# Kernel tuning notes

Hardware: AMD Instinct MI355X
Metric: run time of the kernel (lower is better)

The kernel has to match this reference:

```python
import jax, jax.numpy as jnp
import numpy as np

IN_F = 4096
OUT_F = 4096
RANK = 128  # config.group_size doubles as LoRA rank
B, S = 8, 16


def setup_inputs() -> dict:
    key = jax.random.key(0)
    k_x, k_wq, k_s, k_a, k_b, k_bias = jax.random.split(key, 6)
    x = jax.random.normal(k_x, (B, S, IN_F), dtype=jnp.float32)
    # 4-bit signed quantized weights stored as int8 in torch; int32 here, values in [-8, 7]
    weight_quantized = jax.random.randint(k_wq, (OUT_F, IN_F), -8, 8, dtype=jnp.int32)
    weight_scale = jax.random.uniform(k_s, (OUT_F,), dtype=jnp.float32, minval=0.01, maxval=0.1)
    # kaiming_uniform-ish init for lora_A; lora_B nonzero here so grads flow in tests
    bound = 1.0 / np.sqrt(IN_F)
    lora_A = jax.random.uniform(k_a, (IN_F, RANK), dtype=jnp.float32, minval=-bound, maxval=bound)
    lora_B = jax.random.normal(k_b, (RANK, OUT_F), dtype=jnp.float32) * 0.01
    bias = jax.random.normal(k_bias, (OUT_F,), dtype=jnp.float32) * 0.01
    return {"x": x, "weight_quantized": weight_quantized, "weight_scale": weight_scale,
            "lora_A": lora_A, "lora_B": lora_B, "bias": bias}


def reference(x, weight_quantized, weight_scale, lora_A, lora_B, bias):
    # dequantize: per-output-row scale (out, in)
    weight_dequant = weight_quantized.astype(x.dtype) * weight_scale[:, None]
    # low-rank LoRA update (in, out); square layer so broadcast-add is elementwise
    lora_weight = lora_A @ lora_B
    weight = weight_dequant + lora_weight
    # F.linear: x @ weight.T + bias
    out = jnp.einsum('bsi,oi->bso', x, weight) + bias
    return out
```

## Files before the change

kernel.cpp:

```cpp
#include <hip/hip_runtime.h>
#include <hip/hip_bf16.h>

typedef __attribute__((ext_vector_type(8))) short short8;
typedef __attribute__((ext_vector_type(4))) float f32x4;
using u16 = unsigned short;
using u32 = unsigned int;

#define IN_F 4096
#define OUT_F 4096
#define RANK 128

__device__ inline u32 packi(int a, int b) {
    float fa = (float)a, fb = (float)b;
    return (__builtin_bit_cast(u32, fa) >> 16) |
           (__builtin_bit_cast(u32, fb) & 0xFFFF0000u);
}
__device__ inline u32 packf(float a, float b) {
    u32 ua = __builtin_bit_cast(u32, a);
    u32 ub = __builtin_bit_cast(u32, b);
    ua = (ua + 0x7FFFu + ((ua >> 16) & 1u)) >> 16;
    ub = (ub + 0x7FFFu + ((ub >> 16) & 1u));
    return ua | (ub & 0xFFFF0000u);
}
__device__ inline u16 f2bf(float f) {
    u32 u = __builtin_bit_cast(u32, f);
    u = (u + 0x7FFFu + ((u >> 16) & 1u)) >> 16;
    return (u16)u;
}

#define WS_Y 0
#define WS_YP 65536
#define WS_XB (WS_YP + 1048576)
#define WS_BT (WS_XB + 1048576)
#define WS_AT (WS_BT + 1048576)
#define WS_PART (WS_AT + 1048576)

__global__ __launch_bounds__(512) void prep1_kernel(
    const float* __restrict__ x, const float* __restrict__ A,
    const float* __restrict__ B, u16* __restrict__ xb,
    u16* __restrict__ at, u16* __restrict__ bt) {
    __shared__ float tile[64 * 33];
    int bid = blockIdx.x, tid = threadIdx.x;
    if (bid < 128) {
        const f32x4* xv = (const f32x4*)x;
        int vi = bid * 1024 + tid * 2;
        f32x4 a = xv[vi], b = xv[vi + 1];
        union { u32 u[4]; short8 s; } p;
        p.u[0] = packf(a[0], a[1]); p.u[1] = packf(a[2], a[3]);
        p.u[2] = packf(b[0], b[1]); p.u[3] = packf(b[2], b[3]);
        *(short8*)(xb + (size_t)vi * 4) = p.s;
    } else if (bid < 384) {
        int b2 = bid - 128, kt = b2 >> 2, rt = b2 & 3;
        int k0 = kt * 64, r0 = rt * 32;
        for (int u = tid; u < 2048; u += 512) {
            int row = u >> 5, c = u & 31;
            tile[row * 33 + c] = A[(size_t)(k0 + row) * RANK + r0 + c];
        }
        __syncthreads();
        for (int u = tid; u < 2048; u += 512) {
            int rr = u >> 6, k = u & 63;
            at[(size_t)(r0 + rr) * IN_F + k0 + k] = f2bf(tile[k * 33 + rr]);
        }
    } else {
        int b2 = bid - 384, rt = b2 >> 7, ot = b2 & 127;
        int r0 = rt * 64, o0 = ot * 32;
        for (int u = tid; u < 2048; u += 512) {
            int row = u >> 5, c = u & 31;
            tile[row * 33 + c] = B[(size_t)(r0 + row) * OUT_F + o0 + c];
        }
        __syncthreads();
        for (int u = tid; u < 2048; u += 512) {
            int oo = u >> 6, k = u & 63;
            bt[(size_t)(o0 + oo) * RANK + r0 + k] = f2bf(tile[k * 33 + oo]);
        }
    }
}

__global__ __launch_bounds__(512) void prep2_kernel(
    const u16* __restrict__ xb, const u16* __restrict__ at,
    float* __restrict__ yp) {
    int tid = threadIdx.x, lane = tid & 63, wid = tid >> 6;
    int wm = wid >> 1, wn = wid & 1;
    int col = lane & 15, kg = lane >> 4;
    int rt = blockIdx.x & 3, kq = blockIdx.x >> 2;
    int r = rt * 32 + wn * 16 + col;
    int k0 = kq * 256;
    const u16* xp0 = xb + (size_t)(wm * 32 + col) * IN_F + k0 + kg * 8;
    const u16* xp1 = xp0 + (size_t)16 * IN_F;
    const u16* ap = at + (size_t)r * IN_F + k0 + kg * 8;
    f32x4 acc0 = {0.f, 0.f, 0.f, 0.f}, acc1 = {0.f, 0.f, 0.f, 0.f};
    #pragma unroll
    for (int k = 0; k < 256; k += 32) {
        short8 bf = *(const short8*)(ap + k);
        short8 a0 = *(const short8*)(xp0 + k);
        short8 a1 = *(const short8*)(xp1 + k);
        acc0 = __builtin_amdgcn_mfma_f32_16x16x32_bf16(a0, bf, acc0, 0, 0, 0);
        acc1 = __builtin_amdgcn_mfma_f32_16x16x32_bf16(a1, bf, acc1, 0, 0, 0);
    }
    int rbase = wm * 32 + kg * 4;
    float* yq = yp + (size_t)kq * 128 * RANK;
    #pragma unroll
    for (int j = 0; j < 4; ++j) {
        yq[(rbase + j) * RANK + r] = acc0[j];
        yq[(rbase + j + 16) * RANK + r] = acc1[j];
    }
}

__global__ __launch_bounds__(512) void reduce_y_kernel(
    const float* __restrict__ yp, float* __restrict__ y) {
    int idx = blockIdx.x * 512 + threadIdx.x;
    const f32x4* v = (const f32x4*)yp;
    f32x4 s = {0.f, 0.f, 0.f, 0.f};
    #pragma unroll
    for (int kq = 0; kq < 16; ++kq) {
        f32x4 t = v[kq * 4096 + idx];
        s[0] += t[0]; s[1] += t[1]; s[2] += t[2]; s[3] += t[3];
    }
    ((f32x4*)y)[idx] = s;
}

#define KCHUNK 1024
__global__ __launch_bounds__(512, 4) void main_kernel(
    const u16* __restrict__ xb, const int* __restrict__ wq,
    const float* __restrict__ scale, const float* __restrict__ bias,
    const float* __restrict__ y, const u16* __restrict__ bt,
    float* __restrict__ part) {
    int tid = threadIdx.x, lane = tid & 63, wid = tid >> 6;
    int wm = wid >> 2, wn = wid & 3;
    int col = lane & 15, kg = lane >> 4;
    int bid = blockIdx.x;
    int ot = bid & 63, mt = (bid >> 6) & 1, kq = bid >> 7;
    int o = ot * 64 + wn * 16 + col;
    int m0 = mt * 64 + wm * 32 + col;
    int k0 = kq * KCHUNK;

    const int* wp = wq + (size_t)o * IN_F + k0 + kg * 8;
    const u16* xp0 = xb + (size_t)m0 * IN_F + k0 + kg * 8;
    const u16* xp1 = xp0 + (size_t)16 * IN_F;

    f32x4 acc0 = {0.f, 0.f, 0.f, 0.f}, acc1 = {0.f, 0.f, 0.f, 0.f};
    #pragma unroll 4
    for (int it = 0; it < 32; ++it) {
        int4 wa = *(const int4*)(wp + it * 32);
        int4 wb = *(const int4*)(wp + it * 32 + 4);
        short8 a0 = *(const short8*)(xp0 + it * 32);
        short8 a1 = *(const short8*)(xp1 + it * 32);
        union { u32 u[4]; short8 s; } bf;
        bf.u[0] = packi(wa.x, wa.y); bf.u[1] = packi(wa.z, wa.w);
        bf.u[2] = packi(wb.x, wb.y); bf.u[3] = packi(wb.z, wb.w);
        acc0 = __builtin_amdgcn_mfma_f32_16x16x32_bf16(a0, bf.s, acc0, 0, 0, 0);
        acc1 = __builtin_amdgcn_mfma_f32_16x16x32_bf16(a1, bf.s, acc1, 0, 0, 0);
    }

    float s = scale[o];
    #pragma unroll
    for (int j = 0; j < 4; ++j) { acc0[j] *= s; acc1[j] *= s; }

    if (kq == 0) {
        const float* yp0 = y + (size_t)m0 * RANK + kg * 8;
        const float* yp1 = yp0 + 16 * RANK;
        const u16* bp = bt + (size_t)o * RANK + kg * 8;
        #pragma unroll
        for (int ks = 0; ks < RANK; ks += 32) {
            f32x4 ya = *(const f32x4*)(yp0 + ks);
            f32x4 yb = *(const f32x4*)(yp0 + ks + 4);
            f32x4 yc = *(const f32x4*)(yp1 + ks);
            f32x4 yd = *(const f32x4*)(yp1 + ks + 4);
            union { u32 u[4]; short8 s; } af0, af1;
            af0.u[0] = packf(ya[0], ya[1]); af0.u[1] = packf(ya[2], ya[3]);
            af0.u[2] = packf(yb[0], yb[1]); af0.u[3] = packf(yb[2], yb[3]);
            af1.u[0] = packf(yc[0], yc[1]); af1.u[1] = packf(yc[2], yc[3]);
            af1.u[2] = packf(yd[0], yd[1]); af1.u[3] = packf(yd[2], yd[3]);
            short8 bfr = *(const short8*)(bp + ks);
            acc0 = __builtin_amdgcn_mfma_f32_16x16x32_bf16(af0.s, bfr, acc0, 0, 0, 0);
            acc1 = __builtin_amdgcn_mfma_f32_16x16x32_bf16(af1.s, bfr, acc1, 0, 0, 0);
        }
        float bv = bias[o];
        #pragma unroll
        for (int j = 0; j < 4; ++j) { acc0[j] += bv; acc1[j] += bv; }
    }

    int rbase = mt * 64 + wm * 32 + kg * 4;
    float* op = part + (size_t)kq * 128 * OUT_F + (size_t)rbase * OUT_F + o;
    #pragma unroll
    for (int j = 0; j < 4; ++j) {
        op[(size_t)j * OUT_F] = acc0[j];
        op[(size_t)(j + 16) * OUT_F] = acc1[j];
    }
}

__global__ __launch_bounds__(512) void reduce_out_kernel(
    const float* __restrict__ part, float* __restrict__ out) {
    const f32x4* p0 = (const f32x4*)part;
    const f32x4* p1 = p0 + 131072;
    const f32x4* p2 = p1 + 131072;
    const f32x4* p3 = p2 + 131072;
    f32x4* ov = (f32x4*)out;
    int idx = blockIdx.x * 512 + threadIdx.x;
    f32x4 a = p0[idx], b = p1[idx], c = p2[idx], d = p3[idx];
    f32x4 s;
    #pragma unroll
    for (int j = 0; j < 4; ++j) s[j] = (a[j] + b[j]) + (c[j] + d[j]);
    ov[idx] = s;
}

extern "C" void kernel_launch(void* const* d_in, const int* in_sizes, int n_in,
                              void* d_out, int out_size, void* d_ws, size_t ws_size,
                              hipStream_t stream) {
    const float* x = (const float*)d_in[0];
    const int* wq = (const int*)d_in[1];
    const float* scale = (const float*)d_in[2];
    const float* A = (const float*)d_in[3];
    const float* B = (const float*)d_in[4];
    const float* bias = (const float*)d_in[5];
    float* out = (float*)d_out;

    char* ws = (char*)d_ws;
    float* y = (float*)(ws + WS_Y);
    float* yp = (float*)(ws + WS_YP);
    u16* xb = (u16*)(ws + WS_XB);
    u16* bt = (u16*)(ws + WS_BT);
    u16* at = (u16*)(ws + WS_AT);
    float* part = (float*)(ws + WS_PART);

    prep1_kernel<<<640, 512, 0, stream>>>(x, A, B, xb, at, bt);
    prep2_kernel<<<64, 512, 0, stream>>>(xb, at, yp);
    reduce_y_kernel<<<8, 512, 0, stream>>>(yp, y);
    main_kernel<<<512, 512, 0, stream>>>(xb, wq, scale, bias, y, bt, part);
    reduce_out_kernel<<<256, 512, 0, stream>>>(part, out);
}
```

Baseline: 172.2 us.

## Stage int32 weight tiles through LDS with triple-buffered direct global-to-LDS loads

Replaces the per-thread direct global loads of the int32 weights in the main kernel with a triple-buffered LDS pipeline. It uses global_load_lds asynchronous copies, an XOR swizzle to avoid bank conflicts, and inline-asm prefetch of the bf16 activations one tile ahead. Explicit vmcnt waits and barriers order the stages. The goal is to hide weight-load latency and get coalesced row-contiguous weight fetches, at the cost of 48KB of LDS per block (lower occupancy) and fragile hand-written wait counts and asm.

```diff
diff --git a/kernel.cpp b/kernel.cpp
--- a/kernel.cpp
+++ b/kernel.cpp
@@ -9,6 +9,9 @@
 #define IN_F 4096
 #define OUT_F 4096
 #define RANK 128
+
+typedef const __attribute__((address_space(1))) int* gas_ptr;
+typedef __attribute__((address_space(3))) int* las_ptr;
 
 __device__ inline u32 packi(int a, int b) {
     float fa = (float)a, fb = (float)b;
@@ -119,37 +122,92 @@
     ((f32x4*)y)[idx] = s;
 }
 
-#define KCHUNK 1024
+#define NT 16
+
+#define XLOAD(P, tn) { \
+    const u16* _a = xp0 + (tn) * 64; \
+    const u16* _b = xp1 + (tn) * 64; \
+    asm volatile("global_load_dwordx4 %0, %1, off" : "=v"(x00##P) : "v"(_a)); \
+    asm volatile("global_load_dwordx4 %0, %1, off" : "=v"(x01##P) : "v"(_a + 32)); \
+    asm volatile("global_load_dwordx4 %0, %1, off" : "=v"(x10##P) : "v"(_b)); \
+    asm volatile("global_load_dwordx4 %0, %1, off" : "=v"(x11##P) : "v"(_b + 32)); }
+
+#define STAGE(buf, tt) { \
+    __builtin_amdgcn_global_load_lds((gas_ptr)(sp1 + (tt) * 64), \
+        (las_ptr)&lds[buf][wid * 256], 16, 0, 0); \
+    __builtin_amdgcn_global_load_lds((gas_ptr)(sp2 + (tt) * 64), \
+        (las_ptr)&lds[buf][2048 + wid * 256], 16, 0, 0); }
+
+#define WAITB { \
+    asm volatile("s_waitcnt vmcnt(6)" ::: "memory"); \
+    __builtin_amdgcn_sched_barrier(0); \
+    __builtin_amdgcn_s_barrier(); \
+    __builtin_amdgcn_sched_barrier(0); }
+
+#define COMPUTE(P, t) { \
+    const char* bb = ldsb + ((t) % 3) * 16384 + rbyte; \
+    int4 wa0 = *(const int4*)(bb + ((kg * 32) ^ bx)); \
+    int4 wa1 = *(const int4*)(bb + ((kg * 32 + 16) ^ bx)); \
+    int4 wb0 = *(const int4*)(bb + ((kg * 32 + 128) ^ bx)); \
+    int4 wb1 = *(const int4*)(bb + ((kg * 32 + 144) ^ bx)); \
+    union { u32 u[4]; short8 s; } f0, f1; \
+    f0.u[0] = packi(wa0.x, wa0.y); f0.u[1] = packi(wa0.z, wa0.w); \
+    f0.u[2] = packi(wa1.x, wa1.y); f0.u[3] = packi(wa1.z, wa1.w); \
+    f1.u[0] = packi(wb0.x, wb0.y); f1.u[1] = packi(wb0.z, wb0.w); \
+    f1.u[2] = packi(wb1.x, wb1.y); f1.u[3] = packi(wb1.z, wb1.w); \
+    acc0 = __builtin_amdgcn_mfma_f32_16x16x32_bf16(__builtin_bit_cast(short8, x00##P), f0.s, acc0, 0, 0, 0); \
+    acc1 = __builtin_amdgcn_mfma_f32_16x16x32_bf16(__builtin_bit_cast(short8, x10##P), f0.s, acc1, 0, 0, 0); \
+    acc0 = __builtin_amdgcn_mfma_f32_16x16x32_bf16(__builtin_bit_cast(short8, x01##P), f1.s, acc0, 0, 0, 0); \
+    acc1 = __builtin_amdgcn_mfma_f32_16x16x32_bf16(__builtin_bit_cast(short8, x11##P), f1.s, acc1, 0, 0, 0); }
+
 __global__ __launch_bounds__(512, 4) void main_kernel(
     const u16* __restrict__ xb, const int* __restrict__ wq,
     const float* __restrict__ scale, const float* __restrict__ bias,
     const float* __restrict__ y, const u16* __restrict__ bt,
     float* __restrict__ part) {
+    __shared__ int lds[3][4096];
     int tid = threadIdx.x, lane = tid & 63, wid = tid >> 6;
     int wm = wid >> 2, wn = wid & 3;
     int col = lane & 15, kg = lane >> 4;
     int bid = blockIdx.x;
     int ot = bid & 63, mt = (bid >> 6) & 1, kq = bid >> 7;
-    int o = ot * 64 + wn * 16 + col;
+    int o0 = ot * 64;
+    int o = o0 + wn * 16 + col;
     int m0 = mt * 64 + wm * 32 + col;
-    int k0 = kq * KCHUNK;
-
-    const int* wp = wq + (size_t)o * IN_F + k0 + kg * 8;
+    int k0 = kq * 1024;
+
+    int srow = tid >> 4;
+    int sb = ((tid & 15) * 16) ^ ((srow & 7) << 4);
+    const int* sp1 = wq + (size_t)(o0 + srow) * IN_F + k0 + (sb >> 2);
+    const int* sp2 = wq + (size_t)(o0 + 32 + srow) * IN_F + k0 + (sb >> 2);
+
     const u16* xp0 = xb + (size_t)m0 * IN_F + k0 + kg * 8;
     const u16* xp1 = xp0 + (size_t)16 * IN_F;
 
+    const char* ldsb = (const char*)&lds[0][0];
+    int brow = wn * 16 + col;
+    int rbyte = brow * 256;
+    int bx = (brow & 7) << 4;
+
     f32x4 acc0 = {0.f, 0.f, 0.f, 0.f}, acc1 = {0.f, 0.f, 0.f, 0.f};
-    #pragma unroll 4
-    for (int it = 0; it < 32; ++it) {
-        int4 wa = *(const int4*)(wp + it * 32);
-        int4 wb = *(const int4*)(wp + it * 32 + 4);
-        short8 a0 = *(const short8*)(xp0 + it * 32);
-        short8 a1 = *(const short8*)(xp1 + it * 32);
-        union { u32 u[4]; short8 s; } bf;
-        bf.u[0] = packi(wa.x, wa.y); bf.u[1] = packi(wa.z, wa.w);
-        bf.u[2] = packi(wb.x, wb.y); bf.u[3] = packi(wb.z, wb.w);
-        acc0 = __builtin_amdgcn_mfma_f32_16x16x32_bf16(a0, bf.s, acc0, 0, 0, 0);
-        acc1 = __builtin_amdgcn_mfma_f32_16x16x32_bf16(a1, bf.s, acc1, 0, 0, 0);
+    int4 x00A, x01A, x10A, x11A, x00B, x01B, x10B, x11B;
+
+    STAGE(0, 0)
+    XLOAD(A, 0)
+    STAGE(1, 1)
+    XLOAD(B, 1)
+
+    for (int t = 0; t < NT; t += 2) {
+        int ta = (t + 2 < NT) ? t + 2 : NT - 1;
+        int tb = (t + 3 < NT) ? t + 3 : NT - 1;
+        WAITB;
+        STAGE((t + 2) % 3, ta)
+        COMPUTE(A, t)
+        XLOAD(A, ta)
+        WAITB;
+        STAGE((t + 3) % 3, tb)
+        COMPUTE(B, t + 1)
+        XLOAD(B, tb)
     }
 
     float s = scale[o];
```

New measurement: 152.5 us. -11.4%, faster.
